# Kernel optimization log

Measured on AMD Instinct MI355X. Metric: run time of the kernel, lower is better.

Reference implementation:

```python
import jax, jax.numpy as jnp
import numpy as np

D = 196; NCH = 64; H = 8; DH = 64; INNER = H * DH; MLP = 784; SEQ = 65


def _ln(x, g, b, eps=1e-5):
    m = x.mean(-1, keepdims=True)
    v = x.var(-1, keepdims=True)
    return (x - m) / jnp.sqrt(v + eps) * g + b


def setup_inputs() -> dict:
    key = jax.random.key(0)
    ks = jax.random.split(key, 12)
    f = jax.random.normal
    return dict(
        x=f(ks[0], (1, SEQ, D), dtype=jnp.float32),
        tokens=f(ks[1], (1, D), dtype=jnp.float32),
        x_pe=f(ks[2], (1, NCH, D), dtype=jnp.float32),
        conv_k=f(ks[3], (3, 3), dtype=jnp.float32) * 0.3,   # Conv2d(1,1,3) kernel
        bn_g=jnp.ones(()), bn_b=jnp.zeros(()), bn_rm=jnp.zeros(()), bn_rv=jnp.ones(()),
        fc_w1=f(ks[4], (NCH, 12)) * 0.1,
        fc_w2=f(ks[5], (12, NCH)) * 0.1,
        ln1_g=jnp.ones((D,)), ln1_b=jnp.zeros((D,)),
        ln2_g=jnp.ones((D,)), ln2_b=jnp.zeros((D,)),
        w_qkv=f(ks[6], (D, 3 * INNER)) * 0.05,
        w_out=f(ks[7], (INNER, D)) * 0.05, b_out=jnp.zeros((D,)),
        ff_w1=f(ks[8], (D, MLP)) * 0.05, ff_b1=jnp.zeros((MLP,)),
        ff_w2=f(ks[9], (MLP, D)) * 0.05, ff_b2=jnp.zeros((D,)),
    )


def reference(x, tokens, x_pe, conv_k, bn_g, bn_b, bn_rm, bn_rv,
              fc_w1, fc_w2, ln1_g, ln1_b, ln2_g, ln2_b,
              w_qkv, w_out, b_out, ff_w1, ff_b1, ff_w2, ff_b2):
    # --- per-channel Conv2d(1,1,3,p=1)+BN+ReLU, batched over all 64 rows ---
    # Each row is (1,1,1,196): height 1 with pad 1 means the top/bottom kernel
    # rows only touch zero padding, so only the middle kernel row contributes
    # -> equivalent to a 1D conv with kernel conv_k[1].
    rows = x_pe[0]                      # [64,196]
    km = conv_k[1]                      # [3]
    xp = jnp.pad(rows, ((0, 0), (1, 1)))
    conv = km[0] * xp[:, :D] + km[1] * xp[:, 1:D + 1] + km[2] * xp[:, 2:D + 2]
    bn = (conv - bn_rm) / jnp.sqrt(bn_rv + 1e-5) * bn_g + bn_b
    a = jax.nn.relu(bn)                 # [64,196]  (== x_AfterConv / a)

    # --- sort-based suppress/excitation channel gating ---
    b1 = a.mean(-1)                     # [64] adaptive avg pool
    val = jnp.sort(b1)
    idx = jnp.argsort(b1)
    middle = jnp.where((val.max() < 0) | (val.min() > 0),
                       jnp.int32(32), jnp.argmax(val > 0).astype(jnp.int32))
    rank = jnp.argsort(idx)             # rank of each channel in ascending order
    sup = rank < middle                 # channels in idx[:middle]
    l_s = middle.astype(b1.dtype)
    l_e = (NCH - middle).astype(b1.dtype)
    b2 = jnp.where(sup,
                   b1 - 1.0 / (1.0 + jnp.power(l_s, b1)),
                   b1 + 1.0 / (1.0 + jnp.power(l_e, -b1)))

    c = jax.nn.sigmoid(jax.nn.relu(b2 @ fc_w1) @ fc_w2)   # [64]
    x_att = a * c[:, None]                                  # [64,196]
    x_att = jnp.concatenate([x_att, tokens.reshape(1, D)], axis=0)[None]  # [1,65,196]

    # --- PreNorm attention ---
    h = _ln(x, ln1_g, ln1_b)
    qkv = h @ w_qkv
    q, k, v = jnp.split(qkv, 3, axis=-1)
    def heads(t):
        return t.reshape(1, SEQ, H, DH).transpose(0, 2, 1, 3)  # b h n d
    q, k, v = heads(q), heads(k), heads(v)
    attn = jax.nn.softmax(jnp.einsum('bhnd,bhmd->bhnm', q, k) * (DH ** -0.5), axis=-1)
    o = jnp.einsum('bhnm,bhmd->bhnd', attn, v).transpose(0, 2, 1, 3).reshape(1, SEQ, INNER)
    x = o @ w_out + b_out + x + x_att

    # --- PreNorm feed-forward ---
    h2 = _ln(x, ln2_g, ln2_b)
    x = (jax.nn.gelu(h2 @ ff_w1 + ff_b1, approximate=False) @ ff_w2 + ff_b2) + x
    return x
```

## Files before the change

### kernel.cpp

```cpp
#include <hip/hip_runtime.h>
#include <math.h>

#define D 196
#define NCH 64
#define NH 8
#define DHD 64
#define INNER 512
#define MLP 784
#define SEQ 65

__device__ float g_a[NCH * D];
__device__ float g_b1[NCH];
__device__ float g_qkv[SEQ * 1536];
__device__ float g_x2[SEQ * D];

__device__ __forceinline__ float bsum(float v, float* red) {
    for (int off = 32; off > 0; off >>= 1) v += __shfl_down(v, off, 64);
    int lane = threadIdx.x & 63, wid = threadIdx.x >> 6;
    if (lane == 0) red[wid] = v;
    __syncthreads();
    float s = red[0] + red[1] + red[2] + red[3];
    __syncthreads();
    return s;
}

__global__ void __launch_bounds__(256) k1(const float* __restrict__ x_pe,
        const float* __restrict__ conv_k, const float* __restrict__ bn_g,
        const float* __restrict__ bn_b, const float* __restrict__ bn_rm,
        const float* __restrict__ bn_rv, const float* __restrict__ x,
        const float* __restrict__ ln1_g, const float* __restrict__ ln1_b,
        const float* __restrict__ w_qkv, float* __restrict__ out) {
    __shared__ float red[4];
    __shared__ float h[D];
    __shared__ float ps[512];
    int b = blockIdx.x, t = threadIdx.x;
    if (b < NCH) {
        int zi = b * 200 + t;
        if (t < 200 && zi < SEQ * D) { out[zi] = 0.f; g_x2[zi] = 0.f; }
        const float* row = x_pe + b * D;
        float val = 0.f;
        if (t < D) {
            float km0 = conv_k[3], km1 = conv_k[4], km2 = conv_k[5];
            float inv = rsqrtf(bn_rv[0] + 1e-5f);
            float l = (t > 0) ? row[t - 1] : 0.f;
            float m = row[t];
            float r = (t < D - 1) ? row[t + 1] : 0.f;
            float conv = km0 * l + km1 * m + km2 * r;
            float bn = (conv - bn_rm[0]) * inv * bn_g[0] + bn_b[0];
            val = fmaxf(bn, 0.f);
            g_a[b * D + t] = val;
        }
        float tot = bsum(val, red);
        if (t == 0) g_b1[b] = tot * (1.f / (float)D);
    } else {
        int qb = b - NCH;
        int n = qb / 12, cg = qb % 12;
        const float* row = x + n * D;
        float v = (t < D) ? row[t] : 0.f;
        float mean = bsum(v, red) * (1.f / (float)D);
        float d = (t < D) ? (v - mean) : 0.f;
        float var = bsum(d * d, red) * (1.f / (float)D);
        float rinv = rsqrtf(var + 1e-5f);
        if (t < D) h[t] = d * rinv * ln1_g[t] + ln1_b[t];
        __syncthreads();
        int qq = t >> 6, lt = t & 63;
        int c0 = cg * 128 + lt * 2;
        const float* wp = w_qkv + (qq * 49) * 1536 + c0;
        const float* hp = h + qq * 49;
        float a0 = 0.f, a1 = 0.f;
#pragma unroll
        for (int i = 0; i < 49; i++) {
            float2 w2 = *(const float2*)(wp + i * 1536);
            float hv = hp[i];
            a0 += hv * w2.x;
            a1 += hv * w2.y;
        }
        ps[qq * 128 + lt * 2] = a0;
        ps[qq * 128 + lt * 2 + 1] = a1;
        __syncthreads();
        if (t < 64) {
            float s0 = ps[t * 2] + ps[128 + t * 2] + ps[256 + t * 2] + ps[384 + t * 2];
            float s1 = ps[t * 2 + 1] + ps[129 + t * 2] + ps[257 + t * 2] + ps[385 + t * 2];
            float2 o2 = make_float2(s0, s1);
            *(float2*)(g_qkv + n * 1536 + cg * 128 + t * 2) = o2;
        }
    }
}

__global__ void __launch_bounds__(256) k2(const float* __restrict__ fc_w1,
        const float* __restrict__ fc_w2, const float* __restrict__ w_out,
        const float* __restrict__ b_out, const float* __restrict__ x,
        const float* __restrict__ tokens) {
    __shared__ float sq[128];
    __shared__ float pp[2 * 80];
    __shared__ float so[128];
    __shared__ float ps[784];
    __shared__ float sb1[NCH];
    __shared__ float sb2[NCH];
    __shared__ float hid[12];
    __shared__ float cgate;

    int n = blockIdx.x, g = blockIdx.y, t = threadIdx.x;
    int w = t >> 6, L = t & 63;

    if (t < 128) sq[t] = g_qkv[n * 1536 + g * 128 + t];

    if (g == 0) {
        if (t < NCH) {
            sb1[t] = g_b1[t];
            float v = g_b1[t];
            float mx = -1e30f, mn = 1e30f;
            int cle = 0, rank = 0;
            for (int j = 0; j < NCH; j++) {
                float ww = sb1[j];
                mx = fmaxf(mx, ww);
                mn = fminf(mn, ww);
                if (ww <= 0.f) cle++;
                if (ww < v || (ww == v && j < t)) rank++;
            }
            int middle;
            if (mx < 0.f || mn > 0.f) middle = 32;
            else if (mx <= 0.f) middle = 0;
            else middle = cle;
            float b2;
            if (rank < middle) {
                float ls = (float)middle;
                b2 = v - 1.f / (1.f + powf(ls, v));
            } else {
                float le = (float)(NCH - middle);
                b2 = v + 1.f / (1.f + powf(le, -v));
            }
            sb2[t] = b2;
        }
        if (t < 12) {
            float s = 0.f;
            for (int j = 0; j < NCH; j++) s += sb2[j] * fc_w1[j * 12 + t];
            hid[t] = fmaxf(s, 0.f);
        }
        if (t == 0 && n < NCH) {
            float s = 0.f;
            for (int k = 0; k < 12; k++) s += hid[k] * fc_w2[k * NCH + n];
            cgate = 1.f / (1.f + expf(-s));
        }
    }

    if (t < 128) {
        int head = g * 2 + w;
        const float scale = 0.125f;
        const float4* kr = (const float4*)(g_qkv + L * 1536 + INNER + head * DHD);
        const float4* q4 = (const float4*)(sq + w * DHD);
        float s = 0.f;
#pragma unroll
        for (int i = 0; i < 16; i++) {
            float4 kv = kr[i];
            float4 qv = q4[i];
            s += qv.x * kv.x + qv.y * kv.y + qv.z * kv.z + qv.w * kv.w;
        }
        float sL = s * scale;
        float t64 = sq[w * DHD + L] * g_qkv[64 * 1536 + INNER + head * DHD + L];
#pragma unroll
        for (int off = 1; off < 64; off <<= 1) t64 += __shfl_xor(t64, off, 64);
        float s64 = t64 * scale;
        float mx = sL;
#pragma unroll
        for (int off = 1; off < 64; off <<= 1) mx = fmaxf(mx, __shfl_xor(mx, off, 64));
        mx = fmaxf(mx, s64);
        float e = expf(sL - mx);
        float e64 = expf(s64 - mx);
        float esum = e;
#pragma unroll
        for (int off = 1; off < 64; off <<= 1) esum += __shfl_xor(esum, off, 64);
        esum += e64;
        float rs = 1.f / esum;
        pp[w * 80 + L] = e;
        if (L == 0) pp[w * 80 + 64] = e64;
        float acc = 0.f;
#pragma unroll 13
        for (int m = 0; m < SEQ; m++)
            acc += pp[w * 80 + m] * g_qkv[m * 1536 + 2 * INNER + head * DHD + L];
        so[w * DHD + L] = acc * rs;
    }
    __syncthreads();

    if (t < 196) {
        int qq = t / 49, p = t - qq * 49;
        const float* wp = w_out + (g * 128 + qq * 32) * D + 4 * p;
        const float* op = so + qq * 32;
        float a0 = 0.f, a1 = 0.f, a2 = 0.f, a3 = 0.f;
#pragma unroll
        for (int i = 0; i < 32; i++) {
            float4 w4 = *(const float4*)(wp + i * D);
            float ov = op[i];
            a0 += ov * w4.x;
            a1 += ov * w4.y;
            a2 += ov * w4.z;
            a3 += ov * w4.w;
        }
        ps[qq * 196 + 4 * p]     = a0;
        ps[qq * 196 + 4 * p + 1] = a1;
        ps[qq * 196 + 4 * p + 2] = a2;
        ps[qq * 196 + 4 * p + 3] = a3;
    }
    __syncthreads();
    if (t < 196) {
        float sacc = ps[t] + ps[196 + t] + ps[392 + t] + ps[588 + t];
        if (g == 0) {
            float att = (n < NCH) ? g_a[n * D + t] * cgate : tokens[t];
            sacc += x[n * D + t] + b_out[t] + att;
        }
        atomicAdd(&g_x2[n * D + t], sacc);
    }
}

__global__ void __launch_bounds__(256) k3(const float* __restrict__ ln2_g,
        const float* __restrict__ ln2_b, const float* __restrict__ ff_w1,
        const float* __restrict__ ff_b1, const float* __restrict__ ff_w2,
        const float* __restrict__ ff_b2, float* __restrict__ out) {
    __shared__ float red[4];
    __shared__ float x2s[D];
    __shared__ float h2s[D];
    __shared__ float st[49];
    __shared__ float ps[196];
    int n = blockIdx.x, cg = blockIdx.y, t = threadIdx.x;
    float v = 0.f;
    if (t < D) { v = g_x2[n * D + t]; x2s[t] = v; }
    float mean = bsum(v, red) * (1.f / (float)D);
    float d = (t < D) ? (v - mean) : 0.f;
    float var = bsum(d * d, red) * (1.f / (float)D);
    float rinv = rsqrtf(var + 1e-5f);
    if (t < D) h2s[t] = d * rinv * ln2_g[t] + ln2_b[t];
    __syncthreads();
    if (t < 196) {
        int qq = t / 49, p = t - qq * 49;
        int c0 = cg * 49 + p;
        const float* wp = ff_w1 + (qq * 49) * MLP + c0;
        const float* hp = h2s + qq * 49;
        float a0 = 0.f;
#pragma unroll
        for (int i = 0; i < 49; i++) a0 += hp[i] * wp[i * MLP];
        ps[qq * 49 + p] = a0;
    }
    __syncthreads();
    if (t < 49) {
        float s0 = ps[t] + ps[49 + t] + ps[98 + t] + ps[147 + t] + ff_b1[cg * 49 + t];
        st[t] = 0.5f * s0 * (1.f + erff(s0 * 0.70710678118f));
    }
    __syncthreads();
    if (t < D) {
        const float* wp = ff_w2 + (cg * 49) * D + t;
        float s = 0.f;
#pragma unroll
        for (int i = 0; i < 49; i++) s += st[i] * wp[i * D];
        if (cg == 0) s += ff_b2[t] + x2s[t];
        atomicAdd(&out[n * D + t], s);
    }
}

extern "C" void kernel_launch(void* const* d_in, const int* in_sizes, int n_in,
                              void* d_out, int out_size, void* d_ws, size_t ws_size,
                              hipStream_t stream) {
    const float* x      = (const float*)d_in[0];
    const float* tokens = (const float*)d_in[1];
    const float* x_pe   = (const float*)d_in[2];
    const float* conv_k = (const float*)d_in[3];
    const float* bn_g   = (const float*)d_in[4];
    const float* bn_b   = (const float*)d_in[5];
    const float* bn_rm  = (const float*)d_in[6];
    const float* bn_rv  = (const float*)d_in[7];
    const float* fc_w1  = (const float*)d_in[8];
    const float* fc_w2  = (const float*)d_in[9];
    const float* ln1_g  = (const float*)d_in[10];
    const float* ln1_b  = (const float*)d_in[11];
    const float* ln2_g  = (const float*)d_in[12];
    const float* ln2_b  = (const float*)d_in[13];
    const float* w_qkv  = (const float*)d_in[14];
    const float* w_out  = (const float*)d_in[15];
    const float* b_out  = (const float*)d_in[16];
    const float* ff_w1  = (const float*)d_in[17];
    const float* ff_b1  = (const float*)d_in[18];
    const float* ff_w2  = (const float*)d_in[19];
    const float* ff_b2  = (const float*)d_in[20];
    float* out = (float*)d_out;
    (void)d_ws; (void)ws_size;

    k1<<<844, 256, 0, stream>>>(x_pe, conv_k, bn_g, bn_b, bn_rm, bn_rv,
                                x, ln1_g, ln1_b, w_qkv, out);
    k2<<<dim3(SEQ, 4), 256, 0, stream>>>(fc_w1, fc_w2, w_out, b_out, x, tokens);
    k3<<<dim3(SEQ, 16), 256, 0, stream>>>(ln2_g, ln2_b,
                                          ff_w1, ff_b1, ff_w2, ff_b2, out);
}
```

Before: 124.6 us.

## Fuse attention and feed-forward kernels with per-row counter handoff

Merges the attention/out-projection kernel and the feed-forward kernel into one launch. Attention blocks come first in the grid and bump a per-row atomic counter once their partial sums are added. Feed-forward blocks spin on that counter until all four contributions for their row have arrived. This removes one kernel launch and the device-wide barrier between stages, letting FFN work on early rows overlap attention on later rows. In exchange it relies on lower-indexed blocks being scheduled first, and spinning blocks occupy CU slots while they wait.

```diff
diff --git a/kernel.cpp b/kernel.cpp
--- a/kernel.cpp
+++ b/kernel.cpp
@@ -13,6 +13,7 @@
 __device__ float g_b1[NCH];
 __device__ float g_qkv[SEQ * 1536];
 __device__ float g_x2[SEQ * D];
+__device__ unsigned int g_cnt[SEQ];
 
 __device__ __forceinline__ float bsum(float v, float* red) {
     for (int off = 32; off > 0; off >>= 1) v += __shfl_down(v, off, 64);
@@ -37,6 +38,7 @@
     if (b < NCH) {
         int zi = b * 200 + t;
         if (t < 200 && zi < SEQ * D) { out[zi] = 0.f; g_x2[zi] = 0.f; }
+        if (b == 0 && t < SEQ) g_cnt[t] = 0u;
         const float* row = x_pe + b * D;
         float val = 0.f;
         if (t < D) {
@@ -87,10 +89,13 @@
     }
 }
 
-__global__ void __launch_bounds__(256) k2(const float* __restrict__ fc_w1,
+__global__ void __launch_bounds__(256, 6) k23(const float* __restrict__ fc_w1,
         const float* __restrict__ fc_w2, const float* __restrict__ w_out,
         const float* __restrict__ b_out, const float* __restrict__ x,
-        const float* __restrict__ tokens) {
+        const float* __restrict__ tokens, const float* __restrict__ ln2_g,
+        const float* __restrict__ ln2_b, const float* __restrict__ ff_w1,
+        const float* __restrict__ ff_b1, const float* __restrict__ ff_w2,
+        const float* __restrict__ ff_b2, float* __restrict__ out) {
     __shared__ float sq[128];
     __shared__ float pp[2 * 80];
     __shared__ float so[128];
@@ -99,160 +104,174 @@
     __shared__ float sb2[NCH];
     __shared__ float hid[12];
     __shared__ float cgate;
-
-    int n = blockIdx.x, g = blockIdx.y, t = threadIdx.x;
-    int w = t >> 6, L = t & 63;
-
-    if (t < 128) sq[t] = g_qkv[n * 1536 + g * 128 + t];
-
-    if (g == 0) {
-        if (t < NCH) {
-            sb1[t] = g_b1[t];
-            float v = g_b1[t];
-            float mx = -1e30f, mn = 1e30f;
-            int cle = 0, rank = 0;
-            for (int j = 0; j < NCH; j++) {
-                float ww = sb1[j];
-                mx = fmaxf(mx, ww);
-                mn = fminf(mn, ww);
-                if (ww <= 0.f) cle++;
-                if (ww < v || (ww == v && j < t)) rank++;
-            }
-            int middle;
-            if (mx < 0.f || mn > 0.f) middle = 32;
-            else if (mx <= 0.f) middle = 0;
-            else middle = cle;
-            float b2;
-            if (rank < middle) {
-                float ls = (float)middle;
-                b2 = v - 1.f / (1.f + powf(ls, v));
-            } else {
-                float le = (float)(NCH - middle);
-                b2 = v + 1.f / (1.f + powf(le, -v));
-            }
-            sb2[t] = b2;
-        }
-        if (t < 12) {
-            float s = 0.f;
-            for (int j = 0; j < NCH; j++) s += sb2[j] * fc_w1[j * 12 + t];
-            hid[t] = fmaxf(s, 0.f);
-        }
-        if (t == 0 && n < NCH) {
-            float s = 0.f;
-            for (int k = 0; k < 12; k++) s += hid[k] * fc_w2[k * NCH + n];
-            cgate = 1.f / (1.f + expf(-s));
-        }
-    }
-
-    if (t < 128) {
-        int head = g * 2 + w;
-        const float scale = 0.125f;
-        const float4* kr = (const float4*)(g_qkv + L * 1536 + INNER + head * DHD);
-        const float4* q4 = (const float4*)(sq + w * DHD);
-        float s = 0.f;
-#pragma unroll
-        for (int i = 0; i < 16; i++) {
-            float4 kv = kr[i];
-            float4 qv = q4[i];
-            s += qv.x * kv.x + qv.y * kv.y + qv.z * kv.z + qv.w * kv.w;
-        }
-        float sL = s * scale;
-        float t64 = sq[w * DHD + L] * g_qkv[64 * 1536 + INNER + head * DHD + L];
-#pragma unroll
-        for (int off = 1; off < 64; off <<= 1) t64 += __shfl_xor(t64, off, 64);
-        float s64 = t64 * scale;
-        float mx = sL;
-#pragma unroll
-        for (int off = 1; off < 64; off <<= 1) mx = fmaxf(mx, __shfl_xor(mx, off, 64));
-        mx = fmaxf(mx, s64);
-        float e = expf(sL - mx);
-        float e64 = expf(s64 - mx);
-        float esum = e;
-#pragma unroll
-        for (int off = 1; off < 64; off <<= 1) esum += __shfl_xor(esum, off, 64);
-        esum += e64;
-        float rs = 1.f / esum;
-        pp[w * 80 + L] = e;
-        if (L == 0) pp[w * 80 + 64] = e64;
-        float acc = 0.f;
-#pragma unroll 13
-        for (int m = 0; m < SEQ; m++)
-            acc += pp[w * 80 + m] * g_qkv[m * 1536 + 2 * INNER + head * DHD + L];
-        so[w * DHD + L] = acc * rs;
-    }
-    __syncthreads();
-
-    if (t < 196) {
-        int qq = t / 49, p = t - qq * 49;
-        const float* wp = w_out + (g * 128 + qq * 32) * D + 4 * p;
-        const float* op = so + qq * 32;
-        float a0 = 0.f, a1 = 0.f, a2 = 0.f, a3 = 0.f;
-#pragma unroll
-        for (int i = 0; i < 32; i++) {
-            float4 w4 = *(const float4*)(wp + i * D);
-            float ov = op[i];
-            a0 += ov * w4.x;
-            a1 += ov * w4.y;
-            a2 += ov * w4.z;
-            a3 += ov * w4.w;
-        }
-        ps[qq * 196 + 4 * p]     = a0;
-        ps[qq * 196 + 4 * p + 1] = a1;
-        ps[qq * 196 + 4 * p + 2] = a2;
-        ps[qq * 196 + 4 * p + 3] = a3;
-    }
-    __syncthreads();
-    if (t < 196) {
-        float sacc = ps[t] + ps[196 + t] + ps[392 + t] + ps[588 + t];
-        if (g == 0) {
-            float att = (n < NCH) ? g_a[n * D + t] * cgate : tokens[t];
-            sacc += x[n * D + t] + b_out[t] + att;
-        }
-        atomicAdd(&g_x2[n * D + t], sacc);
-    }
-}
-
-__global__ void __launch_bounds__(256) k3(const float* __restrict__ ln2_g,
-        const float* __restrict__ ln2_b, const float* __restrict__ ff_w1,
-        const float* __restrict__ ff_b1, const float* __restrict__ ff_w2,
-        const float* __restrict__ ff_b2, float* __restrict__ out) {
     __shared__ float red[4];
     __shared__ float x2s[D];
     __shared__ float h2s[D];
     __shared__ float st[49];
-    __shared__ float ps[196];
-    int n = blockIdx.x, cg = blockIdx.y, t = threadIdx.x;
-    float v = 0.f;
-    if (t < D) { v = g_x2[n * D + t]; x2s[t] = v; }
-    float mean = bsum(v, red) * (1.f / (float)D);
-    float d = (t < D) ? (v - mean) : 0.f;
-    float var = bsum(d * d, red) * (1.f / (float)D);
-    float rinv = rsqrtf(var + 1e-5f);
-    if (t < D) h2s[t] = d * rinv * ln2_g[t] + ln2_b[t];
-    __syncthreads();
-    if (t < 196) {
-        int qq = t / 49, p = t - qq * 49;
-        int c0 = cg * 49 + p;
-        const float* wp = ff_w1 + (qq * 49) * MLP + c0;
-        const float* hp = h2s + qq * 49;
-        float a0 = 0.f;
-#pragma unroll
-        for (int i = 0; i < 49; i++) a0 += hp[i] * wp[i * MLP];
-        ps[qq * 49 + p] = a0;
-    }
-    __syncthreads();
-    if (t < 49) {
-        float s0 = ps[t] + ps[49 + t] + ps[98 + t] + ps[147 + t] + ff_b1[cg * 49 + t];
-        st[t] = 0.5f * s0 * (1.f + erff(s0 * 0.70710678118f));
-    }
-    __syncthreads();
-    if (t < D) {
-        const float* wp = ff_w2 + (cg * 49) * D + t;
-        float s = 0.f;
-#pragma unroll
-        for (int i = 0; i < 49; i++) s += st[i] * wp[i * D];
-        if (cg == 0) s += ff_b2[t] + x2s[t];
-        atomicAdd(&out[n * D + t], s);
+    __shared__ float psC[196];
+
+    int b = blockIdx.x, t = threadIdx.x;
+
+    if (b < 260) {
+        int n = b >> 2, g = b & 3;
+        int w = t >> 6, L = t & 63;
+
+        if (t < 128) sq[t] = g_qkv[n * 1536 + g * 128 + t];
+
+        if (g == 0) {
+            if (t < NCH) {
+                sb1[t] = g_b1[t];
+                float v = g_b1[t];
+                float mx = -1e30f, mn = 1e30f;
+                int cle = 0, rank = 0;
+                for (int j = 0; j < NCH; j++) {
+                    float ww = sb1[j];
+                    mx = fmaxf(mx, ww);
+                    mn = fminf(mn, ww);
+                    if (ww <= 0.f) cle++;
+                    if (ww < v || (ww == v && j < t)) rank++;
+                }
+                int middle;
+                if (mx < 0.f || mn > 0.f) middle = 32;
+                else if (mx <= 0.f) middle = 0;
+                else middle = cle;
+                float b2;
+                if (rank < middle) {
+                    float ls = (float)middle;
+                    b2 = v - 1.f / (1.f + powf(ls, v));
+                } else {
+                    float le = (float)(NCH - middle);
+                    b2 = v + 1.f / (1.f + powf(le, -v));
+                }
+                sb2[t] = b2;
+            }
+            if (t < 12) {
+                float s = 0.f;
+                for (int j = 0; j < NCH; j++) s += sb2[j] * fc_w1[j * 12 + t];
+                hid[t] = fmaxf(s, 0.f);
+            }
+            if (t == 0 && n < NCH) {
+                float s = 0.f;
+                for (int k = 0; k < 12; k++) s += hid[k] * fc_w2[k * NCH + n];
+                cgate = 1.f / (1.f + expf(-s));
+            }
+        }
+
+        if (t < 128) {
+            int head = g * 2 + w;
+            const float scale = 0.125f;
+            const float4* kr = (const float4*)(g_qkv + L * 1536 + INNER + head * DHD);
+            const float4* q4 = (const float4*)(sq + w * DHD);
+            float s = 0.f;
+#pragma unroll
+            for (int i = 0; i < 16; i++) {
+                float4 kv = kr[i];
+                float4 qv = q4[i];
+                s += qv.x * kv.x + qv.y * kv.y + qv.z * kv.z + qv.w * kv.w;
+            }
+            float sL = s * scale;
+            float t64 = sq[w * DHD + L] * g_qkv[64 * 1536 + INNER + head * DHD + L];
+#pragma unroll
+            for (int off = 1; off < 64; off <<= 1) t64 += __shfl_xor(t64, off, 64);
+            float s64 = t64 * scale;
+            float mx = sL;
+#pragma unroll
+            for (int off = 1; off < 64; off <<= 1) mx = fmaxf(mx, __shfl_xor(mx, off, 64));
+            mx = fmaxf(mx, s64);
+            float e = expf(sL - mx);
+            float e64 = expf(s64 - mx);
+            float esum = e;
+#pragma unroll
+            for (int off = 1; off < 64; off <<= 1) esum += __shfl_xor(esum, off, 64);
+            esum += e64;
+            float rs = 1.f / esum;
+            pp[w * 80 + L] = e;
+            if (L == 0) pp[w * 80 + 64] = e64;
+            float acc = 0.f;
+#pragma unroll 13
+            for (int m = 0; m < SEQ; m++)
+                acc += pp[w * 80 + m] * g_qkv[m * 1536 + 2 * INNER + head * DHD + L];
+            so[w * DHD + L] = acc * rs;
+        }
+        __syncthreads();
+
+        if (t < 196) {
+            int qq = t / 49, p = t - qq * 49;
+            const float* wp = w_out + (g * 128 + qq * 32) * D + 4 * p;
+            const float* op = so + qq * 32;
+            float a0 = 0.f, a1 = 0.f, a2 = 0.f, a3 = 0.f;
+#pragma unroll
+            for (int i = 0; i < 32; i++) {
+                float4 w4 = *(const float4*)(wp + i * D);
+                float ov = op[i];
+                a0 += ov * w4.x;
+                a1 += ov * w4.y;
+                a2 += ov * w4.z;
+                a3 += ov * w4.w;
+            }
+            ps[qq * 196 + 4 * p]     = a0;
+            ps[qq * 196 + 4 * p + 1] = a1;
+            ps[qq * 196 + 4 * p + 2] = a2;
+            ps[qq * 196 + 4 * p + 3] = a3;
+        }
+        __syncthreads();
+        if (t < 196) {
+            float sacc = ps[t] + ps[196 + t] + ps[392 + t] + ps[588 + t];
+            if (g == 0) {
+                float att = (n < NCH) ? g_a[n * D + t] * cgate : tokens[t];
+                sacc += x[n * D + t] + b_out[t] + att;
+            }
+            atomicAdd(&g_x2[n * D + t], sacc);
+        }
+        __threadfence();
+        __syncthreads();
+        if (t == 0)
+            __hip_atomic_fetch_add(&g_cnt[n], 1u, __ATOMIC_RELEASE,
+                                   __HIP_MEMORY_SCOPE_AGENT);
+    } else {
+        int u = b - 260;
+        int n = u >> 4, fg = u & 15;
+        if (t == 0) {
+            while (__hip_atomic_load(&g_cnt[n], __ATOMIC_RELAXED,
+                                     __HIP_MEMORY_SCOPE_AGENT) < 4u)
+                __builtin_amdgcn_s_sleep(8);
+            (void)__hip_atomic_load(&g_cnt[n], __ATOMIC_ACQUIRE,
+                                    __HIP_MEMORY_SCOPE_AGENT);
+        }
+        __syncthreads();
+
+        float v = 0.f;
+        if (t < D) { v = g_x2[n * D + t]; x2s[t] = v; }
+        float mean = bsum(v, red) * (1.f / (float)D);
+        float d = (t < D) ? (v - mean) : 0.f;
+        float var = bsum(d * d, red) * (1.f / (float)D);
+        float rinv = rsqrtf(var + 1e-5f);
+        if (t < D) h2s[t] = d * rinv * ln2_g[t] + ln2_b[t];
+        __syncthreads();
+        if (t < 196) {
+            int qq = t / 49, p = t - qq * 49;
+            int c0 = fg * 49 + p;
+            const float* wp = ff_w1 + (qq * 49) * MLP + c0;
+            const float* hp = h2s + qq * 49;
+            float a0 = 0.f;
+#pragma unroll
+            for (int i = 0; i < 49; i++) a0 += hp[i] * wp[i * MLP];
+            psC[qq * 49 + p] = a0;
+        }
+        __syncthreads();
+        if (t < 49) {
+            float s0 = psC[t] + psC[49 + t] + psC[98 + t] + psC[147 + t] + ff_b1[fg * 49 + t];
+            st[t] = 0.5f * s0 * (1.f + erff(s0 * 0.70710678118f));
+        }
+        __syncthreads();
+        if (t < D) {
+            const float* wp = ff_w2 + (fg * 49) * D + t;
+            float s = 0.f;
+#pragma unroll
+            for (int i = 0; i < 49; i++) s += st[i] * wp[i * D];
+            if (fg == 0) s += ff_b2[t] + x2s[t];
+            atomicAdd(&out[n * D + t], s);
+        }
     }
 }
 
@@ -285,7 +304,7 @@
 
     k1<<<844, 256, 0, stream>>>(x_pe, conv_k, bn_g, bn_b, bn_rm, bn_rv,
                                 x, ln1_g, ln1_b, w_qkv, out);
-    k2<<<dim3(SEQ, 4), 256, 0, stream>>>(fc_w1, fc_w2, w_out, b_out, x, tokens);
-    k3<<<dim3(SEQ, 16), 256, 0, stream>>>(ln2_g, ln2_b,
-                                          ff_w1, ff_b1, ff_w2, ff_b2, out);
+    k23<<<260 + SEQ * 16, 256, 0, stream>>>(fc_w1, fc_w2, w_out, b_out, x, tokens,
+                                            ln2_g, ln2_b, ff_w1, ff_b1,
+                                            ff_w2, ff_b2, out);
 }
```

Measured after the change: 155.6 us. 1.25x slower.
